# Kernel tuning notes

Measured on AMD Instinct MI355X. Metric: run time of the kernel, lower is better.

Reference implementation:

```python
import jax, jax.numpy as jnp
import numpy as np

SIZE = 512
NUM_HEADS = 8
HEAD_SIZE = SIZE // NUM_HEADS
EPS = 1e-5  # GroupNorm default eps


def setup_inputs() -> dict:
    key = jax.random.key(0)
    ks = jax.random.split(key, 8)
    B, T, D = 2, 2048, SIZE
    mk = lambda k: jax.random.normal(k, (D, D), dtype=jnp.float32) / D
    return {
        "x": jax.random.normal(ks[0], (B, T, D), dtype=jnp.float32),
        "W_Q": mk(ks[1]),
        "W_K": mk(ks[2]),
        "W_V": mk(ks[3]),
        "W_G": mk(ks[4]),
        "W_O": mk(ks[5]),
        "gn_weight": jnp.ones((D,), dtype=jnp.float32),
        "gn_bias": jnp.zeros((D,), dtype=jnp.float32),
    }


def _retention(x, W_Q, W_K, W_V):
    B, T, D = x.shape
    H, dh = NUM_HEADS, HEAD_SIZE
    # projections -> (B, H, T, dh)
    q = (x @ W_Q).reshape(B, T, H, dh).transpose(0, 2, 1, 3)
    k = (x @ W_K).reshape(B, T, H, dh).transpose(0, 2, 1, 3)
    v = (x @ W_V).reshape(B, T, H, dh).transpose(0, 2, 1, 3)
    # multi-scale per-head decay: gamma_h = 1 - 2^{-5-h}
    gammas = 1.0 - jnp.exp2(-5.0 - jnp.arange(H, dtype=jnp.float32))
    idx = jnp.arange(T)
    diff = (idx[:, None] - idx[None, :]).astype(jnp.float32)  # (T, T)
    causal = diff >= 0
    # D[h, n, m] = gamma_h^{n-m} for n >= m else 0
    decay = jnp.where(causal[None], jnp.exp(diff[None] * jnp.log(gammas)[:, None, None]), 0.0)
    scores = jnp.einsum("bhtd,bhsd->bhts", q, k) / jnp.sqrt(jnp.float32(dh))
    out = jnp.einsum("bhts,bhsd->bhtd", scores * decay[None], v)
    return out.transpose(0, 2, 1, 3).reshape(B, T, D)


def _group_norm(y, weight, bias):
    # GroupNorm(NUM_HEADS, SIZE) over flattened (B*T, SIZE)
    B, T, D = y.shape
    g = y.reshape(B * T, NUM_HEADS, HEAD_SIZE)
    mean = jnp.mean(g, axis=-1, keepdims=True)
    var = jnp.var(g, axis=-1, keepdims=True)
    g = (g - mean) / jnp.sqrt(var + EPS)
    g = g.reshape(B * T, D) * weight + bias
    return g.reshape(B, T, D)


def reference(x, W_Q, W_K, W_V, W_G, W_O, gn_weight, gn_bias):
    ret = _retention(x, W_Q, W_K, W_V)          # (B, T, D)
    normed = _group_norm(ret, gn_weight, gn_bias)  # (B, T, D)
    return jax.nn.silu(x @ W_G + normed) @ W_O
```

## Files before the change

### kernel.cpp

```cpp
#include <hip/hip_runtime.h>
#include <hip/hip_bf16.h>
#include <math.h>

#define DMODEL 512
#define T_SEQ 2048
#define NH 8
#define DH 64
#define M_ROWS 4096
#define LDST 72

typedef short s16x8 __attribute__((ext_vector_type(8)));
typedef float f32x4 __attribute__((ext_vector_type(4)));
typedef unsigned short u16x4 __attribute__((ext_vector_type(4)));

static __device__ __forceinline__ unsigned short f2bf(float f) {
  __hip_bfloat16 h = __float2bfloat16(f);
  return *(unsigned short*)&h;
}
static __device__ __forceinline__ float bf2f(unsigned short u) {
  union { unsigned int i; float f; } x; x.i = (unsigned int)u << 16; return x.f;
}

__global__ __launch_bounds__(256) void cast_x_k(
    const float* __restrict__ x, unsigned short* __restrict__ Xb)
{
  const size_t i = ((size_t)blockIdx.x * 256 + threadIdx.x) * 8;
  float4 a = *(const float4*)&x[i];
  float4 b = *(const float4*)&x[i + 4];
  s16x8 o;
  o[0]=f2bf(a.x); o[1]=f2bf(a.y); o[2]=f2bf(a.z); o[3]=f2bf(a.w);
  o[4]=f2bf(b.x); o[5]=f2bf(b.y); o[6]=f2bf(b.z); o[7]=f2bf(b.w);
  *(s16x8*)&Xb[i] = o;
}

__global__ __launch_bounds__(256) void prep_w_k(
    const float* __restrict__ W0, const float* __restrict__ W1,
    const float* __restrict__ W2, const float* __restrict__ W3,
    const float* __restrict__ W4, unsigned short* __restrict__ WT)
{
  __shared__ __align__(16) unsigned short buf[64 * LDST];
  const int n0 = blockIdx.x * 64, k0 = blockIdx.y * 64, z = blockIdx.z;
  const float* W = (z==0)?W0:(z==1)?W1:(z==2)?W2:(z==3)?W3:W4;
  const int tid = threadIdx.x;
  #pragma unroll
  for (int r = 0; r < 4; ++r) {
    int idx = r * 256 + tid;
    int kr = idx >> 4, nc = idx & 15;
    float4 v = *(const float4*)&W[(size_t)(k0 + kr) * DMODEL + n0 + nc * 4];
    buf[(nc*4+0) * LDST + kr] = f2bf(v.x);
    buf[(nc*4+1) * LDST + kr] = f2bf(v.y);
    buf[(nc*4+2) * LDST + kr] = f2bf(v.z);
    buf[(nc*4+3) * LDST + kr] = f2bf(v.w);
  }
  __syncthreads();
  #pragma unroll
  for (int r = 0; r < 2; ++r) {
    int idx = r * 256 + tid;
    int nr = idx >> 3, c = idx & 7;
    *(s16x8*)&WT[((size_t)z * DMODEL + n0 + nr) * DMODEL + k0 + c * 8] =
        *(const s16x8*)&buf[nr * LDST + c * 8];
  }
}

__global__ __launch_bounds__(256) void mfma_gemm_k(
    const unsigned short* __restrict__ A, const unsigned short* __restrict__ BT,
    void* __restrict__ C0, void* __restrict__ C1,
    void* __restrict__ C2, void* __restrict__ C3, int nbf16)
{
  __shared__ __align__(16) unsigned short As[128 * LDST];
  __shared__ __align__(16) unsigned short Bs[128 * LDST];
  const int ng0 = blockIdx.x * 128;
  const int m0 = blockIdx.y * 128;
  const int z = ng0 >> 9, n0 = ng0 & 511;
  void* Cz = (z==0)?C0:(z==1)?C1:(z==2)?C2:C3;
  const int tid = threadIdx.x;
  const int wave = tid >> 6, lane = tid & 63;
  const int wm = wave >> 1, wn = wave & 1;
  const int n = lane & 15, quad = lane >> 4;

  f32x4 acc[4][4];
  #pragma unroll
  for (int mi = 0; mi < 4; ++mi)
    #pragma unroll
    for (int ni = 0; ni < 4; ++ni) acc[mi][ni] = (f32x4){0.f,0.f,0.f,0.f};

  for (int k0 = 0; k0 < 512; k0 += 64) {
    #pragma unroll
    for (int r = 0; r < 4; ++r) {
      int idx = r * 256 + tid;
      int row = idx >> 3, c = idx & 7;
      *(s16x8*)&As[row * LDST + c * 8] =
          *(const s16x8*)&A[(size_t)(m0 + row) * DMODEL + k0 + c * 8];
      *(s16x8*)&Bs[row * LDST + c * 8] =
          *(const s16x8*)&BT[(size_t)(ng0 + row) * DMODEL + k0 + c * 8];
    }
    __syncthreads();
    #pragma unroll
    for (int kk = 0; kk < 2; ++kk) {
      s16x8 af[4], bf[4];
      #pragma unroll
      for (int mi = 0; mi < 4; ++mi)
        af[mi] = *(const s16x8*)&As[(wm*64 + mi*16 + n) * LDST + kk*32 + quad*8];
      #pragma unroll
      for (int ni = 0; ni < 4; ++ni)
        bf[ni] = *(const s16x8*)&Bs[(wn*64 + ni*16 + n) * LDST + kk*32 + quad*8];
      #pragma unroll
      for (int mi = 0; mi < 4; ++mi)
        #pragma unroll
        for (int ni = 0; ni < 4; ++ni)
          acc[mi][ni] = __builtin_amdgcn_mfma_f32_16x16x32_bf16(
              af[mi], bf[ni], acc[mi][ni], 0, 0, 0);
    }
    __syncthreads();
  }

  if (z < nbf16) {
    unsigned short* Cb = (unsigned short*)Cz;
    #pragma unroll
    for (int mi = 0; mi < 4; ++mi)
      #pragma unroll
      for (int ni = 0; ni < 4; ++ni)
        #pragma unroll
        for (int r = 0; r < 4; ++r)
          Cb[(size_t)(m0 + wm*64 + mi*16 + quad*4 + r) * DMODEL +
             n0 + wn*64 + ni*16 + n] = f2bf(acc[mi][ni][r]);
  } else {
    float* Cf = (float*)Cz;
    #pragma unroll
    for (int mi = 0; mi < 4; ++mi)
      #pragma unroll
      for (int ni = 0; ni < 4; ++ni)
        #pragma unroll
        for (int r = 0; r < 4; ++r)
          Cf[(size_t)(m0 + wm*64 + mi*16 + quad*4 + r) * DMODEL +
             n0 + wn*64 + ni*16 + n] = acc[mi][ni][r];
  }
}

__global__ __launch_bounds__(256) void ret_kv_k(
    const unsigned short* __restrict__ Kb, const unsigned short* __restrict__ Vb,
    float* __restrict__ AT)
{
  __shared__ __align__(16) unsigned short Kts[64 * LDST];
  __shared__ __align__(16) unsigned short Vts[64 * LDST];
  const int c = blockIdx.x, h = blockIdx.y, b = blockIdx.z;
  const int bh = b * NH + h;
  const int tid = threadIdx.x;
  const int wave = tid >> 6, lane = tid & 63;
  const int n = lane & 15, quad = lane >> 4;
  const size_t base = ((size_t)b * T_SEQ + (size_t)c * 64) * DMODEL + h * DH;
  const float lg = log2f(1.0f - exp2f(-5.0f - (float)h));

  #pragma unroll
  for (int r = 0; r < 2; ++r) {
    int idx = r * 256 + tid;
    int m = idx & 63, ch = idx >> 6;
    s16x8 kv = *(const s16x8*)&Kb[base + (size_t)m * DMODEL + ch * 8];
    s16x8 vv = *(const s16x8*)&Vb[base + (size_t)m * DMODEL + ch * 8];
    float sc = exp2f((float)(64 - m) * lg);
    #pragma unroll
    for (int e = 0; e < 8; ++e) {
      Kts[(ch * 8 + e) * LDST + m] = f2bf(bf2f(((unsigned short*)&kv)[e]) * sc);
      Vts[(ch * 8 + e) * LDST + m] = ((unsigned short*)&vv)[e];
    }
  }
  __syncthreads();

  f32x4 at[4];
  #pragma unroll
  for (int j = 0; j < 4; ++j) at[j] = (f32x4){0.f,0.f,0.f,0.f};
  #pragma unroll
  for (int kk = 0; kk < 2; ++kk) {
    s16x8 a = *(const s16x8*)&Vts[(wave*16 + n) * LDST + kk*32 + quad*8];
    #pragma unroll
    for (int j = 0; j < 4; ++j) {
      s16x8 bf = *(const s16x8*)&Kts[(j*16 + n) * LDST + kk*32 + quad*8];
      at[j] = __builtin_amdgcn_mfma_f32_16x16x32_bf16(a, bf, at[j], 0, 0, 0);
    }
  }
  float* Ab = AT + (((size_t)bh * 32 + c) << 12);
  #pragma unroll
  for (int j = 0; j < 4; ++j)
    #pragma unroll
    for (int r = 0; r < 4; ++r)
      Ab[(wave*16 + quad*4 + r) * 64 + j*16 + n] = at[j][r];
}

__global__ __launch_bounds__(256) void ret_scan_k(
    const float* __restrict__ AT, unsigned short* __restrict__ St)
{
  const int q = blockIdx.x, bh = blockIdx.y;
  const float lg = log2f(1.0f - exp2f(-5.0f - (float)(bh & 7)));
  const float g64 = exp2f(64.0f * lg);
  const size_t eoff = (size_t)q * 1024 + (size_t)threadIdx.x * 4;
  const float* Ab = AT + (((size_t)bh * 32) << 12) + eoff;
  unsigned short* Sb = St + (((size_t)bh * 32) << 12) + eoff;
  float4 S = make_float4(0.f, 0.f, 0.f, 0.f);
  float4 nxt = *(const float4*)Ab;
  for (int c = 0; c < 32; ++c) {
    float4 a = nxt;
    if (c < 31) nxt = *(const float4*)(Ab + ((size_t)(c + 1) << 12));
    u16x4 o;
    o[0] = f2bf(S.x); o[1] = f2bf(S.y); o[2] = f2bf(S.z); o[3] = f2bf(S.w);
    *(u16x4*)(Sb + ((size_t)c << 12)) = o;
    S.x = fmaf(g64, S.x, a.x); S.y = fmaf(g64, S.y, a.y);
    S.z = fmaf(g64, S.z, a.z); S.w = fmaf(g64, S.w, a.w);
  }
}

__global__ __launch_bounds__(256) void ret_o_k(
    const unsigned short* __restrict__ Qb, const unsigned short* __restrict__ Kb,
    const unsigned short* __restrict__ Vb, const unsigned short* __restrict__ St,
    float* __restrict__ RET)
{
  __shared__ __align__(16) unsigned short Qs[64 * LDST];
  __shared__ __align__(16) unsigned short Ks[64 * LDST];
  __shared__ __align__(16) unsigned short Vst[64 * LDST];
  __shared__ __align__(16) unsigned short Ss[64 * LDST];
  __shared__ __align__(16) unsigned short Ps[64 * LDST];
  const int c = blockIdx.x, h = blockIdx.y, b = blockIdx.z;
  const int bh = b * NH + h;
  const int tid = threadIdx.x;
  const int wave = tid >> 6, lane = tid & 63;
  const int n = lane & 15, quad = lane >> 4;
  const size_t base = ((size_t)b * T_SEQ + (size_t)c * 64) * DMODEL + h * DH;
  const unsigned short* Sg = St + (((size_t)bh * 32 + c) << 12);
  const float lg = log2f(1.0f - exp2f(-5.0f - (float)h));

  #pragma unroll
  for (int r = 0; r < 2; ++r) {
    int idx = r * 256 + tid;
    int i = idx >> 3, ch = idx & 7;
    *(s16x8*)&Qs[i * LDST + ch * 8] =
        *(const s16x8*)&Qb[base + (size_t)i * DMODEL + ch * 8];
    *(s16x8*)&Ks[i * LDST + ch * 8] =
        *(const s16x8*)&Kb[base + (size_t)i * DMODEL + ch * 8];
    *(s16x8*)&Ss[i * LDST + ch * 8] = *(const s16x8*)&Sg[i * 64 + ch * 8];
  }
  #pragma unroll
  for (int r = 0; r < 2; ++r) {
    int idx = r * 256 + tid;
    int m = idx & 63, ch = idx >> 6;
    s16x8 vv = *(const s16x8*)&Vb[base + (size_t)m * DMODEL + ch * 8];
    #pragma unroll
    for (int e = 0; e < 8; ++e)
      Vst[(ch * 8 + e) * LDST + m] = ((unsigned short*)&vv)[e];
  }
  __syncthreads();

  f32x4 s[4], u[4];
  #pragma unroll
  for (int j = 0; j < 4; ++j) {
    s[j] = (f32x4){0.f,0.f,0.f,0.f};
    u[j] = (f32x4){0.f,0.f,0.f,0.f};
  }
  #pragma unroll
  for (int kk = 0; kk < 2; ++kk) {
    s16x8 a = *(const s16x8*)&Qs[(wave*16 + n) * LDST + kk*32 + quad*8];
    #pragma unroll
    for (int j = 0; j < 4; ++j) {
      s16x8 bk = *(const s16x8*)&Ks[(j*16 + n) * LDST + kk*32 + quad*8];
      s[j] = __builtin_amdgcn_mfma_f32_16x16x32_bf16(a, bk, s[j], 0, 0, 0);
      s16x8 bs = *(const s16x8*)&Ss[(j*16 + n) * LDST + kk*32 + quad*8];
      u[j] = __builtin_amdgcn_mfma_f32_16x16x32_bf16(a, bs, u[j], 0, 0, 0);
    }
  }

  float rowf[4], colf[4];
  #pragma unroll
  for (int r = 0; r < 4; ++r) rowf[r] = exp2f((float)(wave*16 + quad*4 + r) * lg);
  #pragma unroll
  for (int j = 0; j < 4; ++j) colf[j] = exp2f(-(float)(j*16 + n) * lg);

  #pragma unroll
  for (int j = 0; j < 4; ++j)
    #pragma unroll
    for (int r = 0; r < 4; ++r) {
      int i = wave*16 + quad*4 + r, mcol = j*16 + n;
      float v = (mcol <= i) ? s[j][r] * 0.125f * rowf[r] * colf[j] : 0.0f;
      Ps[i * LDST + mcol] = f2bf(v);
    }
  __syncthreads();

  f32x4 acc[4];
  #pragma unroll
  for (int j = 0; j < 4; ++j) acc[j] = (f32x4){0.f,0.f,0.f,0.f};
  #pragma unroll
  for (int kk = 0; kk < 2; ++kk) {
    s16x8 a = *(const s16x8*)&Ps[(wave*16 + n) * LDST + kk*32 + quad*8];
    #pragma unroll
    for (int j = 0; j < 4; ++j) {
      s16x8 bf = *(const s16x8*)&Vst[(j*16 + n) * LDST + kk*32 + quad*8];
      acc[j] = __builtin_amdgcn_mfma_f32_16x16x32_bf16(a, bf, acc[j], 0, 0, 0);
    }
  }

  #pragma unroll
  for (int j = 0; j < 4; ++j)
    #pragma unroll
    for (int r = 0; r < 4; ++r) {
      int i = wave*16 + quad*4 + r;
      RET[((size_t)b * T_SEQ + (size_t)c * 64 + i) * DMODEL + h*DH + j*16 + n] =
          acc[j][r] + 0.125f * rowf[r] * u[j][r];
    }
}

__global__ __launch_bounds__(512) void gn_gate_k(
    const float* __restrict__ RET, const float* __restrict__ Gg,
    const float* __restrict__ gw, const float* __restrict__ gb,
    unsigned short* __restrict__ S)
{
  const int row = blockIdx.x;
  const int tid = threadIdx.x;
  const float r = RET[(size_t)row * DMODEL + tid];
  float sum = r, sq = r * r;
  #pragma unroll
  for (int off = 32; off > 0; off >>= 1) {
    sum += __shfl_xor(sum, off, 64);
    sq  += __shfl_xor(sq,  off, 64);
  }
  const float mean = sum * (1.0f / 64.0f);
  float var = sq * (1.0f / 64.0f) - mean * mean;
  var = fmaxf(var, 0.0f);
  const float rstd = rsqrtf(var + 1e-5f);
  const float normed = (r - mean) * rstd * gw[tid] + gb[tid];
  const float u = Gg[(size_t)row * DMODEL + tid] + normed;
  S[(size_t)row * DMODEL + tid] = f2bf(u / (1.0f + expf(-u)));
}

extern "C" void kernel_launch(void* const* d_in, const int* in_sizes, int n_in,
                              void* d_out, int out_size, void* d_ws, size_t ws_size,
                              hipStream_t stream) {
  const float* x   = (const float*)d_in[0];
  const float* WQ  = (const float*)d_in[1];
  const float* WK  = (const float*)d_in[2];
  const float* WV  = (const float*)d_in[3];
  const float* WG  = (const float*)d_in[4];
  const float* WO  = (const float*)d_in[5];
  const float* gnw = (const float*)d_in[6];
  const float* gnb = (const float*)d_in[7];
  float* out = (float*)d_out;

  char* ws = (char*)d_ws;
  unsigned short* Xb = (unsigned short*)(ws);
  unsigned short* Qb = (unsigned short*)(ws + 4  * (1<<20));
  unsigned short* Kb = (unsigned short*)(ws + 8  * (1<<20));
  unsigned short* Vb = (unsigned short*)(ws + 12 * (1<<20));
  float* G   = (float*)(ws + 16 * (1<<20));
  float* AT  = (float*)(ws + 24 * (1<<20));
  float* RET = AT;
  unsigned short* Sb = (unsigned short*)(ws + 32 * (1<<20));
  unsigned short* WT = (unsigned short*)(ws + 36 * (1<<20));
  unsigned short* St = (unsigned short*)(ws + 40 * (1<<20));
  (void)ws_size;

  cast_x_k<<<dim3(M_ROWS * DMODEL / (256 * 8)), 256, 0, stream>>>(x, Xb);
  prep_w_k<<<dim3(8, 8, 5), 256, 0, stream>>>(WQ, WK, WV, WG, WO, WT);
  mfma_gemm_k<<<dim3(16, M_ROWS / 128), 256, 0, stream>>>(
      Xb, WT, Qb, Kb, Vb, G, 3);
  ret_kv_k<<<dim3(T_SEQ / 64, NH, 2), 256, 0, stream>>>(Kb, Vb, AT);
  ret_scan_k<<<dim3(4, 16), 256, 0, stream>>>(AT, St);
  ret_o_k<<<dim3(T_SEQ / 64, NH, 2), 256, 0, stream>>>(Qb, Kb, Vb, St, RET);
  gn_gate_k<<<dim3(M_ROWS), 512, 0, stream>>>(RET, G, gnw, gnb, Sb);
  mfma_gemm_k<<<dim3(4, M_ROWS / 128), 256, 0, stream>>>(
      Sb, WT + 4 * DMODEL * DMODEL, out, out, out, out, 0);
}
```

Before: 128.4 us.

## Merge prep kernels, use direct-to-LDS loads with XOR swizzle, store gate in bf16

Merges the x cast and weight transpose kernels into one launch. In the GEMM, staging goes through global_load_lds 16-byte direct-to-LDS loads into an unpadded, XOR-swizzled tile instead of register round-trips into a padded layout. The gate projection output is now written as bf16 rather than fp32, and the groupnorm/gate kernel reads it as bf16. This saves a launch, some register traffic and gate memory bandwidth, at the cost of lower precision in the gate term and a dependence on the direct-to-LDS builtin and its lane addressing being correct.

Result: no change. 126.5 us (-1.4%).

```diff
diff --git a/kernel.cpp b/kernel.cpp
--- a/kernel.cpp
+++ b/kernel.cpp
@@ -20,28 +20,34 @@
 static __device__ __forceinline__ float bf2f(unsigned short u) {
   union { unsigned int i; float f; } x; x.i = (unsigned int)u << 16; return x.f;
 }
-
-__global__ __launch_bounds__(256) void cast_x_k(
-    const float* __restrict__ x, unsigned short* __restrict__ Xb)
-{
-  const size_t i = ((size_t)blockIdx.x * 256 + threadIdx.x) * 8;
-  float4 a = *(const float4*)&x[i];
-  float4 b = *(const float4*)&x[i + 4];
-  s16x8 o;
-  o[0]=f2bf(a.x); o[1]=f2bf(a.y); o[2]=f2bf(a.z); o[3]=f2bf(a.w);
-  o[4]=f2bf(b.x); o[5]=f2bf(b.y); o[6]=f2bf(b.z); o[7]=f2bf(b.w);
-  *(s16x8*)&Xb[i] = o;
-}
-
-__global__ __launch_bounds__(256) void prep_w_k(
+static __device__ __forceinline__ void gld16(void* lds, const void* g) {
+  __builtin_amdgcn_global_load_lds(
+      (const __attribute__((address_space(1))) unsigned int*)g,
+      (__attribute__((address_space(3))) unsigned int*)lds, 16, 0, 0);
+}
+
+__global__ __launch_bounds__(256) void prep_k(
+    const float* __restrict__ x, unsigned short* __restrict__ Xb,
     const float* __restrict__ W0, const float* __restrict__ W1,
     const float* __restrict__ W2, const float* __restrict__ W3,
     const float* __restrict__ W4, unsigned short* __restrict__ WT)
 {
   __shared__ __align__(16) unsigned short buf[64 * LDST];
-  const int n0 = blockIdx.x * 64, k0 = blockIdx.y * 64, z = blockIdx.z;
+  const int bid = blockIdx.x, tid = threadIdx.x;
+  if (bid < 1024) {
+    const size_t i = ((size_t)bid * 256 + tid) * 8;
+    float4 a = *(const float4*)&x[i];
+    float4 b = *(const float4*)&x[i + 4];
+    s16x8 o;
+    o[0]=f2bf(a.x); o[1]=f2bf(a.y); o[2]=f2bf(a.z); o[3]=f2bf(a.w);
+    o[4]=f2bf(b.x); o[5]=f2bf(b.y); o[6]=f2bf(b.z); o[7]=f2bf(b.w);
+    *(s16x8*)&Xb[i] = o;
+    return;
+  }
+  const int bid2 = bid - 1024;
+  const int z = bid2 >> 6, rem = bid2 & 63;
+  const int n0 = (rem & 7) * 64, k0 = (rem >> 3) * 64;
   const float* W = (z==0)?W0:(z==1)?W1:(z==2)?W2:(z==3)?W3:W4;
-  const int tid = threadIdx.x;
   #pragma unroll
   for (int r = 0; r < 4; ++r) {
     int idx = r * 256 + tid;
@@ -67,8 +73,8 @@
     void* __restrict__ C0, void* __restrict__ C1,
     void* __restrict__ C2, void* __restrict__ C3, int nbf16)
 {
-  __shared__ __align__(16) unsigned short As[128 * LDST];
-  __shared__ __align__(16) unsigned short Bs[128 * LDST];
+  __shared__ __align__(16) unsigned short As[128 * 64];
+  __shared__ __align__(16) unsigned short Bs[128 * 64];
   const int ng0 = blockIdx.x * 128;
   const int m0 = blockIdx.y * 128;
   const int z = ng0 >> 9, n0 = ng0 & 511;
@@ -78,6 +84,14 @@
   const int wm = wave >> 1, wn = wave & 1;
   const int n = lane & 15, quad = lane >> 4;
 
+  int srow[4], scol[4];
+  #pragma unroll
+  for (int r = 0; r < 4; ++r) {
+    int idx = r * 256 + tid;
+    srow[r] = idx >> 3;
+    scol[r] = ((idx & 7) ^ (srow[r] & 7)) * 8;
+  }
+
   f32x4 acc[4][4];
   #pragma unroll
   for (int mi = 0; mi < 4; ++mi)
@@ -88,22 +102,23 @@
     #pragma unroll
     for (int r = 0; r < 4; ++r) {
       int idx = r * 256 + tid;
-      int row = idx >> 3, c = idx & 7;
-      *(s16x8*)&As[row * LDST + c * 8] =
-          *(const s16x8*)&A[(size_t)(m0 + row) * DMODEL + k0 + c * 8];
-      *(s16x8*)&Bs[row * LDST + c * 8] =
-          *(const s16x8*)&BT[(size_t)(ng0 + row) * DMODEL + k0 + c * 8];
+      gld16(&As[idx * 8], &A[(size_t)(m0 + srow[r]) * DMODEL + k0 + scol[r]]);
+      gld16(&Bs[idx * 8], &BT[(size_t)(ng0 + srow[r]) * DMODEL + k0 + scol[r]]);
     }
     __syncthreads();
     #pragma unroll
     for (int kk = 0; kk < 2; ++kk) {
       s16x8 af[4], bf[4];
       #pragma unroll
-      for (int mi = 0; mi < 4; ++mi)
-        af[mi] = *(const s16x8*)&As[(wm*64 + mi*16 + n) * LDST + kk*32 + quad*8];
-      #pragma unroll
-      for (int ni = 0; ni < 4; ++ni)
-        bf[ni] = *(const s16x8*)&Bs[(wn*64 + ni*16 + n) * LDST + kk*32 + quad*8];
+      for (int mi = 0; mi < 4; ++mi) {
+        int R = wm*64 + mi*16 + n, cc = (kk*4 + quad) ^ (n & 7);
+        af[mi] = *(const s16x8*)&As[R * 64 + cc * 8];
+      }
+      #pragma unroll
+      for (int ni = 0; ni < 4; ++ni) {
+        int R = wn*64 + ni*16 + n, cc = (kk*4 + quad) ^ (n & 7);
+        bf[ni] = *(const s16x8*)&Bs[R * 64 + cc * 8];
+      }
       #pragma unroll
       for (int mi = 0; mi < 4; ++mi)
         #pragma unroll
@@ -306,7 +321,7 @@
 }
 
 __global__ __launch_bounds__(512) void gn_gate_k(
-    const float* __restrict__ RET, const float* __restrict__ Gg,
+    const float* __restrict__ RET, const unsigned short* __restrict__ Gg,
     const float* __restrict__ gw, const float* __restrict__ gb,
     unsigned short* __restrict__ S)
 {
@@ -324,7 +339,7 @@
   var = fmaxf(var, 0.0f);
   const float rstd = rsqrtf(var + 1e-5f);
   const float normed = (r - mean) * rstd * gw[tid] + gb[tid];
-  const float u = Gg[(size_t)row * DMODEL + tid] + normed;
+  const float u = bf2f(Gg[(size_t)row * DMODEL + tid]) + normed;
   S[(size_t)row * DMODEL + tid] = f2bf(u / (1.0f + expf(-u)));
 }
 
@@ -346,7 +361,7 @@
   unsigned short* Qb = (unsigned short*)(ws + 4  * (1<<20));
   unsigned short* Kb = (unsigned short*)(ws + 8  * (1<<20));
   unsigned short* Vb = (unsigned short*)(ws + 12 * (1<<20));
-  float* G   = (float*)(ws + 16 * (1<<20));
+  unsigned short* G  = (unsigned short*)(ws + 16 * (1<<20));
   float* AT  = (float*)(ws + 24 * (1<<20));
   float* RET = AT;
   unsigned short* Sb = (unsigned short*)(ws + 32 * (1<<20));
@@ -354,10 +369,9 @@
   unsigned short* St = (unsigned short*)(ws + 40 * (1<<20));
   (void)ws_size;
 
-  cast_x_k<<<dim3(M_ROWS * DMODEL / (256 * 8)), 256, 0, stream>>>(x, Xb);
-  prep_w_k<<<dim3(8, 8, 5), 256, 0, stream>>>(WQ, WK, WV, WG, WO, WT);
+  prep_k<<<dim3(1024 + 320), 256, 0, stream>>>(x, Xb, WQ, WK, WV, WG, WO, WT);
   mfma_gemm_k<<<dim3(16, M_ROWS / 128), 256, 0, stream>>>(
-      Xb, WT, Qb, Kb, Vb, G, 3);
+      Xb, WT, Qb, Kb, Vb, G, 4);
   ret_kv_k<<<dim3(T_SEQ / 64, NH, 2), 256, 0, stream>>>(Kb, Vb, AT);
   ret_scan_k<<<dim3(4, 16), 256, 0, stream>>>(AT, St);
   ret_o_k<<<dim3(T_SEQ / 64, NH, 2), 256, 0, stream>>>(Qb, Kb, Vb, St, RET);
```
